# Kernel optimization log

Measured on AMD Instinct MI355X. Metric: run time of the kernel, lower is better.

## Reference

```python
import jax, jax.numpy as jnp
import numpy as np

N = 50000
IN_C, HID_C, OUT_C = 128, 64, 32
E = 800000
NEG_SLOPE = 0.2


def setup_inputs() -> dict:
    key = jax.random.key(0)
    ks = jax.random.split(key, 8)
    x = jax.random.normal(ks[0], (N, IN_C), dtype=jnp.float32)
    edge_index = jax.random.randint(ks[1], (2, E), 0, N, dtype=jnp.int64)
    # GATConv params (heads=1): lin weight, att_src/att_dst vectors, bias
    sc = 1.0 / np.sqrt(IN_C)
    W = jax.random.uniform(ks[2], (IN_C, HID_C), jnp.float32, -sc, sc)
    att_src = jax.random.normal(ks[3], (HID_C,), jnp.float32) * (1.0 / np.sqrt(HID_C))
    att_dst = jax.random.normal(ks[4], (HID_C,), jnp.float32) * (1.0 / np.sqrt(HID_C))
    bias_conv = jnp.zeros((HID_C,), jnp.float32)
    sl = 1.0 / np.sqrt(HID_C)
    W_lin = jax.random.uniform(ks[5], (HID_C, OUT_C), jnp.float32, -sl, sl)
    b_lin = jax.random.uniform(ks[6], (OUT_C,), jnp.float32, -sl, sl)
    return {"x": x, "edge_index": edge_index, "W": W, "att_src": att_src,
            "att_dst": att_dst, "bias_conv": bias_conv, "W_lin": W_lin, "b_lin": b_lin}


def reference(x, edge_index, W, att_src, att_dst, bias_conv, W_lin, b_lin):
    n = x.shape[0]
    h = x @ W  # [N, HID]
    # add self-loops (PyG GATConv default add_self_loops=True)
    loop = jnp.arange(n, dtype=edge_index.dtype)
    src = jnp.concatenate([edge_index[0], loop])  # [E+N]
    dst = jnp.concatenate([edge_index[1], loop])
    a_src = h @ att_src  # [N]
    a_dst = h @ att_dst
    e = jax.nn.leaky_relu(a_src[src] + a_dst[dst], NEG_SLOPE)  # [E+N]
    # segment softmax over incoming edges per destination node
    m = jax.ops.segment_max(e, dst, num_segments=n)
    e = jnp.exp(e - m[dst])
    denom = jax.ops.segment_sum(e, dst, num_segments=n)
    alpha = e / (denom[dst] + 1e-16)
    msg = alpha[:, None] * h[src]  # [E+N, HID]
    out = jax.ops.segment_sum(msg, dst, num_segments=n) + bias_conv
    out = jax.nn.relu(out)
    return out @ W_lin + b_lin
```

## Files before the change

### kernel.cpp

```cpp
#include <hip/hip_runtime.h>
#include <hip/hip_bf16.h>

#define IN_C  128
#define HID_C 64
#define OUT_C 32
#define NEG_SLOPE 0.2f
#define EPB1    4096
#define BUCKETW 64
#define RCAP    1536
#define NBKT    1024
#define CSTRIDE 16
#define XS_LD   136

typedef short bf16x8 __attribute__((ext_vector_type(8)));
typedef float f32x4  __attribute__((ext_vector_type(4)));

__device__ __forceinline__ unsigned short f2bf(float f) {
    __hip_bfloat16 h = __float2bfloat16(f);
    return *(unsigned short*)&h;
}
__device__ __forceinline__ float bflo(unsigned int u) {
    return __uint_as_float(u << 16);
}
__device__ __forceinline__ float bfhi(unsigned int u) {
    return __uint_as_float(u & 0xffff0000u);
}

__global__ __launch_bounds__(512) void gemm_bin1_kernel(
    const float* __restrict__ x, const float* __restrict__ W,
    const float* __restrict__ att_src, const float* __restrict__ att_dst,
    __hip_bfloat16* __restrict__ hb,
    float* __restrict__ a_src, float* __restrict__ a_dst,
    const int* __restrict__ ei, int E,
    int* __restrict__ bcur, unsigned* __restrict__ bucketbuf,
    int ngemm, int n_nodes)
{
    __shared__ __align__(16) unsigned char smem[52224];
    const int t = threadIdx.x;

    if ((int)blockIdx.x < ngemm) {
        unsigned short* xs = (unsigned short*)smem;
        unsigned short* wt = (unsigned short*)(smem + 34816);
        const int wv   = t >> 6;
        const int lane = t & 63;
        const int m16  = lane & 15;
        const int quad = lane >> 4;
        const int node0 = blockIdx.x * 128;
        const int nrows = min(128, n_nodes - node0);

        {
            const float4* xg = (const float4*)(x + (long)node0 * IN_C);
#pragma unroll
            for (int i = t; i < 4096; i += 512) {
                const int row = i >> 5;
                const int c4  = i & 31;
                float4 v = (row < nrows) ? xg[i] : make_float4(0.f, 0.f, 0.f, 0.f);
                ushort4 u;
                u.x = f2bf(v.x); u.y = f2bf(v.y);
                u.z = f2bf(v.z); u.w = f2bf(v.w);
                *(ushort4*)(xs + row * XS_LD + c4 * 4) = u;
            }
        }
        {
#pragma unroll
            for (int i = t; i < 2048; i += 512) {
                const int k  = i >> 4;
                const int n0 = (i & 15) * 4;
                const float4 v = *(const float4*)(W + k * HID_C + n0);
                wt[(n0 + 0) * XS_LD + k] = f2bf(v.x);
                wt[(n0 + 1) * XS_LD + k] = f2bf(v.y);
                wt[(n0 + 2) * XS_LD + k] = f2bf(v.z);
                wt[(n0 + 3) * XS_LD + k] = f2bf(v.w);
            }
        }
        __syncthreads();

        const int myrow0 = wv * 16;
        bf16x8 A[4];
#pragma unroll
        for (int k0 = 0; k0 < 4; ++k0)
            A[k0] = *(const bf16x8*)(xs + (myrow0 + m16) * XS_LD + k0 * 32 + quad * 8);

        f32x4 C[4];
#pragma unroll
        for (int c = 0; c < 4; ++c) {
            C[c] = (f32x4){0.f, 0.f, 0.f, 0.f};
#pragma unroll
            for (int k0 = 0; k0 < 4; ++k0) {
                const bf16x8 B = *(const bf16x8*)(wt + (c * 16 + m16) * XS_LD + k0 * 32 + quad * 8);
                C[c] = __builtin_amdgcn_mfma_f32_16x16x32_bf16(A[k0], B, C[c], 0, 0, 0);
            }
        }

#pragma unroll
        for (int c = 0; c < 4; ++c) {
#pragma unroll
            for (int r = 0; r < 4; ++r)
                xs[(myrow0 + quad * 4 + r) * XS_LD + c * 16 + m16] = f2bf(C[c][r]);
        }

        {
            float ps[4] = {0.f, 0.f, 0.f, 0.f};
            float pd[4] = {0.f, 0.f, 0.f, 0.f};
#pragma unroll
            for (int c = 0; c < 4; ++c) {
                const float av = att_src[c * 16 + m16];
                const float dv = att_dst[c * 16 + m16];
#pragma unroll
                for (int r = 0; r < 4; ++r) {
                    ps[r] = fmaf(C[c][r], av, ps[r]);
                    pd[r] = fmaf(C[c][r], dv, pd[r]);
                }
            }
#pragma unroll
            for (int off = 1; off <= 8; off <<= 1) {
#pragma unroll
                for (int r = 0; r < 4; ++r) {
                    ps[r] += __shfl_xor(ps[r], off, 64);
                    pd[r] += __shfl_xor(pd[r], off, 64);
                }
            }
            if (m16 == 0) {
#pragma unroll
                for (int r = 0; r < 4; ++r) {
                    const int row = myrow0 + quad * 4 + r;
                    if (row < nrows) {
                        a_src[node0 + row] = ps[r];
                        a_dst[node0 + row] = pd[r];
                    }
                }
            }
        }
        __syncthreads();

        {
#pragma unroll
            for (int i = t; i < 1024; i += 512) {
                const int row = i >> 3;
                const int c8  = (i & 7) * 8;
                if (row < nrows) {
                    const uint4 v = *(const uint4*)(xs + row * XS_LD + c8);
                    *(uint4*)((unsigned short*)hb + (long)(node0 + row) * HID_C + c8) = v;
                }
            }
        }
    } else {
        unsigned* stage = (unsigned*)smem;
        int* excl = (int*)(smem + 16384);
        int* cur  = (int*)(smem + 20480);
        int* gpos = (int*)(smem + 24576);
        int* wsum = (int*)(smem + 28672);

        const int base = (blockIdx.x - ngemm) * EPB1;
        const int nedge = min(EPB1, E - base);
        const int lane = t & 63, wv = t >> 6;

        for (int i = t; i < NBKT; i += 512) excl[i] = 0;
        __syncthreads();

        for (int i = t; i < nedge; i += 512)
            atomicAdd(&excl[ei[E + base + i] >> 6], 1);
        __syncthreads();

        {
            const int b0 = t * 2;
            const int c0 = excl[b0], c1 = excl[b0 + 1];
            const int tsum = c0 + c1;
            int incl = tsum;
#pragma unroll
            for (int off = 1; off <= 32; off <<= 1) {
                int u = __shfl_up(incl, off, 64);
                if (lane >= off) incl += u;
            }
            if (lane == 63) wsum[wv] = incl;
            __syncthreads();
            int wbase = 0;
#pragma unroll
            for (int w = 0; w < 8; ++w) wbase += (w < wv) ? wsum[w] : 0;
            int run = wbase + (incl - tsum);
            excl[b0]     = run; cur[b0]     = run; run += c0;
            excl[b0 + 1] = run; cur[b0 + 1] = run;
        }
        __syncthreads();

        for (int i = t; i < nedge; i += 512) {
            const int s = ei[base + i];
            const int d = ei[E + base + i];
            const int b = d >> 6;
            const int pos = atomicAdd(&cur[b], 1);
            stage[pos] = (unsigned)s | ((unsigned)(d & 63) << 16)
                         | ((unsigned)b << 22);
        }
        __syncthreads();

        for (int b = t; b < NBKT; b += 512) {
            const int c = cur[b] - excl[b];
            gpos[b] = (c > 0) ? atomicAdd(&bcur[b * CSTRIDE], c) : 0;
        }
        __syncthreads();

        for (int i = t; i < nedge; i += 512) {
            const unsigned r = stage[i];
            const int b = r >> 22;
            const int dp = gpos[b] + (i - excl[b]);
            if (dp < RCAP) bucketbuf[(long)b * RCAP + dp] = r & 0x3FFFFFu;
        }
    }
}

__global__ __launch_bounds__(512) void weight_kernel(
    const unsigned* __restrict__ bucketbuf, const int* __restrict__ bcursor,
    const float* __restrict__ a_src, const float* __restrict__ a_dst,
    float* __restrict__ wbuf)
{
    const int t = threadIdx.x;
    const int q = blockIdx.x;
    const int d0 = q * BUCKETW;
    const int tot = min(bcursor[q * CSTRIDE], RCAP);
    const unsigned* src = bucketbuf + (long)q * RCAP;
    float* wdst = wbuf + (long)q * RCAP;

    const int i0 = t, i1 = t + 512, i2 = t + 1024;
    const bool v0 = i0 < tot, v1 = i1 < tot, v2 = i2 < tot;
    const unsigned r0 = v0 ? src[i0] : 0u;
    const unsigned r1 = v1 ? src[i1] : 0u;
    const unsigned r2 = v2 ? src[i2] : 0u;
    const float as0 = v0 ? a_src[r0 & 0xFFFF] : 0.f;
    const float as1 = v1 ? a_src[r1 & 0xFFFF] : 0.f;
    const float as2 = v2 ? a_src[r2 & 0xFFFF] : 0.f;
    const float ad0 = v0 ? a_dst[d0 + ((r0 >> 16) & 63)] : 0.f;
    const float ad1 = v1 ? a_dst[d0 + ((r1 >> 16) & 63)] : 0.f;
    const float ad2 = v2 ? a_dst[d0 + ((r2 >> 16) & 63)] : 0.f;
    if (v0) { float e = as0 + ad0; e = (e >= 0.f) ? e : NEG_SLOPE * e; wdst[i0] = __expf(e); }
    if (v1) { float e = as1 + ad1; e = (e >= 0.f) ? e : NEG_SLOPE * e; wdst[i1] = __expf(e); }
    if (v2) { float e = as2 + ad2; e = (e >= 0.f) ? e : NEG_SLOPE * e; wdst[i2] = __expf(e); }
}

__global__ __launch_bounds__(512) void bucket_agg_kernel(
    const unsigned* __restrict__ bucketbuf, const float* __restrict__ wbuf,
    const int* __restrict__ bcursor,
    const __hip_bfloat16* __restrict__ hb,
    const float* __restrict__ a_src, const float* __restrict__ a_dst,
    const float* __restrict__ bias_conv,
    const float* __restrict__ W_lin, const float* __restrict__ b_lin,
    float* __restrict__ out, int n_nodes)
{
    __shared__ unsigned srtL[RCAP];
    __shared__ float    srtW[RCAP];
    __shared__ int cntd[BUCKETW];
    __shared__ int rp[BUCKETW + 1];
    __shared__ int curd[BUCKETW];

    const int t  = threadIdx.x;
    const int q  = blockIdx.x;
    const int d0 = q * BUCKETW;
    const int dmax = min(BUCKETW, n_nodes - d0);
    const int tot  = min(bcursor[q * CSTRIDE], RCAP);
    const int wv = t >> 6, lane = t & 63, g8 = lane >> 3, l = lane & 7;

    if (t < BUCKETW) cntd[t] = 0;
    __syncthreads();

    const unsigned* gsrc = bucketbuf + (long)q * RCAP;
    const float*    wsrc = wbuf + (long)q * RCAP;

    const int i0 = t, i1 = t + 512, i2 = t + 1024;
    const bool v0 = i0 < tot, v1 = i1 < tot, v2 = i2 < tot;
    const unsigned rr0 = v0 ? gsrc[i0] : 0u;
    const unsigned rr1 = v1 ? gsrc[i1] : 0u;
    const unsigned rr2 = v2 ? gsrc[i2] : 0u;
    const float    ww0 = v0 ? wsrc[i0] : 0.f;
    const float    ww1 = v1 ? wsrc[i1] : 0.f;
    const float    ww2 = v2 ? wsrc[i2] : 0.f;

    if (v0) atomicAdd(&cntd[(rr0 >> 16) & 63], 1);
    if (v1) atomicAdd(&cntd[(rr1 >> 16) & 63], 1);
    if (v2) atomicAdd(&cntd[(rr2 >> 16) & 63], 1);
    __syncthreads();

    if (t < 64) {
        int c = cntd[t], incl = c;
#pragma unroll
        for (int off = 1; off <= 32; off <<= 1) {
            int u = __shfl_up(incl, off, 64);
            if (t >= off) incl += u;
        }
        rp[t] = incl - c;
        curd[t] = incl - c;
        if (t == 63) rp[64] = incl;
    }
    __syncthreads();

    if (v0) { const int p = atomicAdd(&curd[(rr0 >> 16) & 63], 1); srtL[p] = rr0; srtW[p] = ww0; }
    if (v1) { const int p = atomicAdd(&curd[(rr1 >> 16) & 63], 1); srtL[p] = rr1; srtW[p] = ww1; }
    if (v2) { const int p = atomicAdd(&curd[(rr2 >> 16) & 63], 1); srtL[p] = rr2; srtW[p] = ww2; }
    __syncthreads();

    float Wr[8][4];
#pragma unroll
    for (int kc = 0; kc < 8; ++kc)
#pragma unroll
        for (int kj = 0; kj < 4; ++kj)
            Wr[kc][kj] = W_lin[(l * 8 + kc) * OUT_C + g8 * 4 + kj];
    float biasR[8];
#pragma unroll
    for (int kc = 0; kc < 8; ++kc) biasR[kc] = bias_conv[l * 8 + kc];
    float blinR[4];
#pragma unroll
    for (int kj = 0; kj < 4; ++kj) blinR[kj] = b_lin[g8 * 4 + kj];

    const unsigned short* hbs = (const unsigned short*)hb;

    for (int dloc = wv; dloc < dmax; dloc += 8) {
        const int d = d0 + dloc;
        float A[8] = {0.f,0.f,0.f,0.f,0.f,0.f,0.f,0.f};
        float den = 0.f;
        if (g8 == 0) {
            float e = a_src[d] + a_dst[d];
            e = (e >= 0.f) ? e : NEG_SLOPE * e;
            const float ws = __expf(e);
            const uint4 hv = *(const uint4*)(hbs + (long)d * HID_C + l * 8);
            den = ws;
            A[0] = ws * bflo(hv.x); A[1] = ws * bfhi(hv.x);
            A[2] = ws * bflo(hv.y); A[3] = ws * bfhi(hv.y);
            A[4] = ws * bflo(hv.z); A[5] = ws * bfhi(hv.z);
            A[6] = ws * bflo(hv.w); A[7] = ws * bfhi(hv.w);
        }
        const int beg = rp[dloc], fin = rp[dloc + 1];
        for (int j = beg + g8; j < fin; j += 16) {
            const int  j1   = j + 8;
            const bool has1 = j1 < fin;
            const int  j1c  = has1 ? j1 : j;
            const unsigned r0 = srtL[j];
            const unsigned r1 = srtL[j1c];
            const float w0 = srtW[j];
            const float w1 = has1 ? srtW[j1c] : 0.f;
            const int   s0 = r0 & 0xFFFF;
            const int   s1 = r1 & 0xFFFF;
            const uint4 h0 = *(const uint4*)(hbs + (long)s0 * HID_C + l * 8);
            const uint4 h1 = *(const uint4*)(hbs + (long)s1 * HID_C + l * 8);
            den += w0 + w1;
            A[0] = fmaf(w0, bflo(h0.x), A[0]); A[1] = fmaf(w0, bfhi(h0.x), A[1]);
            A[2] = fmaf(w0, bflo(h0.y), A[2]); A[3] = fmaf(w0, bfhi(h0.y), A[3]);
            A[4] = fmaf(w0, bflo(h0.z), A[4]); A[5] = fmaf(w0, bfhi(h0.z), A[5]);
            A[6] = fmaf(w0, bflo(h0.w), A[6]); A[7] = fmaf(w0, bfhi(h0.w), A[7]);
            A[0] = fmaf(w1, bflo(h1.x), A[0]); A[1] = fmaf(w1, bfhi(h1.x), A[1]);
            A[2] = fmaf(w1, bflo(h1.y), A[2]); A[3] = fmaf(w1, bfhi(h1.y), A[3]);
            A[4] = fmaf(w1, bflo(h1.z), A[4]); A[5] = fmaf(w1, bfhi(h1.z), A[5]);
            A[6] = fmaf(w1, bflo(h1.w), A[6]); A[7] = fmaf(w1, bfhi(h1.w), A[7]);
        }
#pragma unroll
        for (int off = 8; off <= 32; off <<= 1) {
#pragma unroll
            for (int k = 0; k < 8; ++k) A[k] += __shfl_xor(A[k], off, 64);
            den += __shfl_xor(den, off, 64);
        }
        const float rd = 1.0f / (den + 1e-16f);
        float p0 = 0.f, p1 = 0.f, p2 = 0.f, p3 = 0.f;
#pragma unroll
        for (int kc = 0; kc < 8; ++kc) {
            float vv = fmaf(A[kc], rd, biasR[kc]);
            vv = vv > 0.f ? vv : 0.f;
            p0 = fmaf(vv, Wr[kc][0], p0);
            p1 = fmaf(vv, Wr[kc][1], p1);
            p2 = fmaf(vv, Wr[kc][2], p2);
            p3 = fmaf(vv, Wr[kc][3], p3);
        }
#pragma unroll
        for (int off = 1; off <= 4; off <<= 1) {
            p0 += __shfl_xor(p0, off, 64);
            p1 += __shfl_xor(p1, off, 64);
            p2 += __shfl_xor(p2, off, 64);
            p3 += __shfl_xor(p3, off, 64);
        }
        if (l == 0) {
            float4 o = make_float4(p0 + blinR[0], p1 + blinR[1],
                                   p2 + blinR[2], p3 + blinR[3]);
            *(float4*)(out + (long)d * OUT_C + g8 * 4) = o;
        }
    }
}

extern "C" void kernel_launch(void* const* d_in, const int* in_sizes, int n_in,
                              void* d_out, int out_size, void* d_ws, size_t ws_size,
                              hipStream_t stream) {
    const float* x         = (const float*)d_in[0];
    const int*   ei        = (const int*)d_in[1];
    const float* W         = (const float*)d_in[2];
    const float* att_src   = (const float*)d_in[3];
    const float* att_dst   = (const float*)d_in[4];
    const float* bias_conv = (const float*)d_in[5];
    const float* W_lin     = (const float*)d_in[6];
    const float* b_lin     = (const float*)d_in[7];
    float*       out       = (float*)d_out;

    const int n_nodes = in_sizes[0] / IN_C;
    const int E       = in_sizes[1] / 2;
    const int B1   = (E + EPB1 - 1) / EPB1;
    const int Q    = (n_nodes + BUCKETW - 1) / BUCKETW;
    const int NG   = (n_nodes + 127) / 128;

    __hip_bfloat16* hb = (__hip_bfloat16*)d_ws;
    float* a_src   = (float*)(hb + (long)n_nodes * HID_C);
    float* a_dst   = a_src + n_nodes;
    int*   bcur    = (int*)(a_dst + n_nodes);
    unsigned* bucketbuf = (unsigned*)(bcur + (long)Q * CSTRIDE);
    float* wbuf    = (float*)(bucketbuf + (long)Q * RCAP);

    hipMemsetAsync(bcur, 0, (size_t)Q * CSTRIDE * sizeof(int), stream);

    gemm_bin1_kernel<<<NG + B1, 512, 0, stream>>>(
        x, W, att_src, att_dst, hb, a_src, a_dst,
        ei, E, bcur, bucketbuf, NG, n_nodes);

    weight_kernel<<<Q, 512, 0, stream>>>(
        bucketbuf, bcur, a_src, a_dst, wbuf);

    bucket_agg_kernel<<<Q, 512, 0, stream>>>(
        bucketbuf, wbuf, bcur, hb, a_src, a_dst,
        bias_conv, W_lin, b_lin, out, n_nodes);
}
```

Baseline: 155.3 us.

## Assign one destination node per 8-lane group and stage ReLU activations in LDS

The aggregation loop now gives each 8-lane group its own destination node and walks that node's edges sequentially, instead of one wavefront cooperating on a node and reducing across lane groups with shuffles. The post-ReLU hidden vectors are written to shared memory, which reuses the sort buffers, and a second phase performs the 64x32 linear projection per node. This removes the cross-group shuffle reductions and the idle lanes on low-degree nodes. In exchange it adds two block barriers and shared-memory traffic, and lanes diverge when neighbouring nodes have different degrees.

Result: faster. 138.5 us (-10.8%).

```diff
diff --git a/kernel.cpp b/kernel.cpp
--- a/kernel.cpp
+++ b/kernel.cpp
@@ -245,11 +245,13 @@
     const float* __restrict__ W_lin, const float* __restrict__ b_lin,
     float* __restrict__ out, int n_nodes)
 {
-    __shared__ unsigned srtL[RCAP];
-    __shared__ float    srtW[RCAP];
-    __shared__ int cntd[BUCKETW];
-    __shared__ int rp[BUCKETW + 1];
-    __shared__ int curd[BUCKETW];
+    __shared__ __align__(16) unsigned char smem[16384];
+    unsigned* srtL = (unsigned*)smem;
+    float*    srtW = (float*)(smem + 6144);
+    int* cntd = (int*)(smem + 12288);
+    int* rp   = (int*)(smem + 12544);
+    int* curd = (int*)(smem + 12804);
+    float* vvL = (float*)smem;
 
     const int t  = threadIdx.x;
     const int q  = blockIdx.x;
@@ -296,26 +298,18 @@
     if (v2) { const int p = atomicAdd(&curd[(rr2 >> 16) & 63], 1); srtL[p] = rr2; srtW[p] = ww2; }
     __syncthreads();
 
-    float Wr[8][4];
-#pragma unroll
-    for (int kc = 0; kc < 8; ++kc)
-#pragma unroll
-        for (int kj = 0; kj < 4; ++kj)
-            Wr[kc][kj] = W_lin[(l * 8 + kc) * OUT_C + g8 * 4 + kj];
-    float biasR[8];
-#pragma unroll
-    for (int kc = 0; kc < 8; ++kc) biasR[kc] = bias_conv[l * 8 + kc];
-    float blinR[4];
-#pragma unroll
-    for (int kj = 0; kj < 4; ++kj) blinR[kj] = b_lin[g8 * 4 + kj];
-
     const unsigned short* hbs = (const unsigned short*)hb;
 
-    for (int dloc = wv; dloc < dmax; dloc += 8) {
+    const int dloc = wv * 8 + g8;
+    float vv[8];
+#pragma unroll
+    for (int kc = 0; kc < 8; ++kc) vv[kc] = 0.f;
+
+    if (dloc < dmax) {
         const int d = d0 + dloc;
-        float A[8] = {0.f,0.f,0.f,0.f,0.f,0.f,0.f,0.f};
-        float den = 0.f;
-        if (g8 == 0) {
+        float A[8];
+        float den;
+        {
             float e = a_src[d] + a_dst[d];
             e = (e >= 0.f) ? e : NEG_SLOPE * e;
             const float ws = __expf(e);
@@ -327,18 +321,14 @@
             A[6] = ws * bflo(hv.w); A[7] = ws * bfhi(hv.w);
         }
         const int beg = rp[dloc], fin = rp[dloc + 1];
-        for (int j = beg + g8; j < fin; j += 16) {
-            const int  j1   = j + 8;
-            const bool has1 = j1 < fin;
-            const int  j1c  = has1 ? j1 : j;
+        int j = beg;
+        for (; j + 1 < fin; j += 2) {
             const unsigned r0 = srtL[j];
-            const unsigned r1 = srtL[j1c];
-            const float w0 = srtW[j];
-            const float w1 = has1 ? srtW[j1c] : 0.f;
-            const int   s0 = r0 & 0xFFFF;
-            const int   s1 = r1 & 0xFFFF;
-            const uint4 h0 = *(const uint4*)(hbs + (long)s0 * HID_C + l * 8);
-            const uint4 h1 = *(const uint4*)(hbs + (long)s1 * HID_C + l * 8);
+            const unsigned r1 = srtL[j + 1];
+            const float    w0 = srtW[j];
+            const float    w1 = srtW[j + 1];
+            const uint4 h0 = *(const uint4*)(hbs + (long)(r0 & 0xFFFF) * HID_C + l * 8);
+            const uint4 h1 = *(const uint4*)(hbs + (long)(r1 & 0xFFFF) * HID_C + l * 8);
             den += w0 + w1;
             A[0] = fmaf(w0, bflo(h0.x), A[0]); A[1] = fmaf(w0, bfhi(h0.x), A[1]);
             A[2] = fmaf(w0, bflo(h0.y), A[2]); A[3] = fmaf(w0, bfhi(h0.y), A[3]);
@@ -349,22 +339,51 @@
             A[4] = fmaf(w1, bflo(h1.z), A[4]); A[5] = fmaf(w1, bfhi(h1.z), A[5]);
             A[6] = fmaf(w1, bflo(h1.w), A[6]); A[7] = fmaf(w1, bfhi(h1.w), A[7]);
         }
-#pragma unroll
-        for (int off = 8; off <= 32; off <<= 1) {
-#pragma unroll
-            for (int k = 0; k < 8; ++k) A[k] += __shfl_xor(A[k], off, 64);
-            den += __shfl_xor(den, off, 64);
+        if (j < fin) {
+            const unsigned r0 = srtL[j];
+            const float    w0 = srtW[j];
+            const uint4 h0 = *(const uint4*)(hbs + (long)(r0 & 0xFFFF) * HID_C + l * 8);
+            den += w0;
+            A[0] = fmaf(w0, bflo(h0.x), A[0]); A[1] = fmaf(w0, bfhi(h0.x), A[1]);
+            A[2] = fmaf(w0, bflo(h0.y), A[2]); A[3] = fmaf(w0, bfhi(h0.y), A[3]);
+            A[4] = fmaf(w0, bflo(h0.z), A[4]); A[5] = fmaf(w0, bfhi(h0.z), A[5]);
+            A[6] = fmaf(w0, bflo(h0.w), A[6]); A[7] = fmaf(w0, bfhi(h0.w), A[7]);
         }
         const float rd = 1.0f / (den + 1e-16f);
+#pragma unroll
+        for (int kc = 0; kc < 8; ++kc) {
+            float v = fmaf(A[kc], rd, bias_conv[l * 8 + kc]);
+            vv[kc] = v > 0.f ? v : 0.f;
+        }
+    }
+
+    __syncthreads();
+
+    *(float4*)(vvL + dloc * HID_C + l * 8)     = make_float4(vv[0], vv[1], vv[2], vv[3]);
+    *(float4*)(vvL + dloc * HID_C + l * 8 + 4) = make_float4(vv[4], vv[5], vv[6], vv[7]);
+    __syncthreads();
+
+    float Wr[8][4];
+#pragma unroll
+    for (int kc = 0; kc < 8; ++kc)
+#pragma unroll
+        for (int kj = 0; kj < 4; ++kj)
+            Wr[kc][kj] = W_lin[(l * 8 + kc) * OUT_C + g8 * 4 + kj];
+    float blinR[4];
+#pragma unroll
+    for (int kj = 0; kj < 4; ++kj) blinR[kj] = b_lin[g8 * 4 + kj];
+
+    for (int dl = wv; dl < dmax; dl += 8) {
+        const float4 va = *(const float4*)(vvL + dl * HID_C + l * 8);
+        const float4 vb = *(const float4*)(vvL + dl * HID_C + l * 8 + 4);
+        const float vvr[8] = {va.x, va.y, va.z, va.w, vb.x, vb.y, vb.z, vb.w};
         float p0 = 0.f, p1 = 0.f, p2 = 0.f, p3 = 0.f;
 #pragma unroll
         for (int kc = 0; kc < 8; ++kc) {
-            float vv = fmaf(A[kc], rd, biasR[kc]);
-            vv = vv > 0.f ? vv : 0.f;
-            p0 = fmaf(vv, Wr[kc][0], p0);
-            p1 = fmaf(vv, Wr[kc][1], p1);
-            p2 = fmaf(vv, Wr[kc][2], p2);
-            p3 = fmaf(vv, Wr[kc][3], p3);
+            p0 = fmaf(vvr[kc], Wr[kc][0], p0);
+            p1 = fmaf(vvr[kc], Wr[kc][1], p1);
+            p2 = fmaf(vvr[kc], Wr[kc][2], p2);
+            p3 = fmaf(vvr[kc], Wr[kc][3], p3);
         }
 #pragma unroll
         for (int off = 1; off <= 4; off <<= 1) {
@@ -376,7 +395,7 @@
         if (l == 0) {
             float4 o = make_float4(p0 + blinR[0], p1 + blinR[1],
                                    p2 + blinR[2], p3 + blinR[3]);
-            *(float4*)(out + (long)d * OUT_C + g8 * 4) = o;
+            *(float4*)(out + (long)(d0 + dl) * OUT_C + g8 * 4) = o;
         }
     }
 }
```
